# Kernel optimization log

Measured on AMD Instinct MI355X. Metric: run time of the kernel, lower is better.

Reference implementation:

```python
import jax, jax.numpy as jnp
import numpy as np

NEG = -1e30  # log-space 'zero' that stays finite under autodiff
BLANK = 0


def _logsumexp3(a, b, c):
    m = jnp.maximum(jnp.maximum(a, b), c)
    return m + jnp.log(jnp.exp(a - m) + jnp.exp(b - m) + jnp.exp(c - m))


def setup_inputs() -> dict:
    key = jax.random.key(0)
    k1, k2, k3, k4 = jax.random.split(key, 4)
    T, B, C, S = 1024, 128, 96, 200
    logits = jax.random.normal(k1, (T, B, C), dtype=jnp.float32)
    log_probs = jax.nn.log_softmax(logits, axis=-1)  # CTC expects log-probs
    targets = jax.random.randint(k2, (B, S), 1, C, dtype=jnp.int32)  # labels in [1, C-1]
    input_lengths = jax.random.randint(k3, (B,), T // 2, T + 1, dtype=jnp.int32)
    target_lengths = jax.random.randint(k4, (B,), S // 2, S + 1, dtype=jnp.int32)
    return {"log_probs": log_probs, "targets": targets,
            "input_lengths": input_lengths, "target_lengths": target_lengths}


def ctc_loss(log_probs, targets, input_lengths, target_lengths):
    T, B, C = log_probs.shape
    S = targets.shape[1]
    L = 2 * S + 1  # extended target length (blanks interleaved)

    # Extended target sequence: blank, t0, blank, t1, ..., blank  -> [B, L]
    ext = jnp.zeros((B, L), dtype=targets.dtype).at[:, 1::2].set(targets)
    # Skip transition s-2 -> s allowed when ext[s] != blank and ext[s] != ext[s-2]
    ext_m2 = jnp.pad(ext[:, :-2], ((0, 0), (2, 0)), constant_values=BLANK)
    allow_skip = (ext != BLANK) & (ext != ext_m2) & (jnp.arange(L)[None, :] >= 2)

    emit0 = jnp.take_along_axis(log_probs[0], ext, axis=1)  # [B, L]
    alpha0 = jnp.full((B, L), NEG, dtype=log_probs.dtype)
    alpha0 = alpha0.at[:, 0].set(emit0[:, 0]).at[:, 1].set(emit0[:, 1])

    def step(alpha, lp_t):
        a1 = jnp.pad(alpha[:, :-1], ((0, 0), (1, 0)), constant_values=NEG)
        a2 = jnp.pad(alpha[:, :-2], ((0, 0), (2, 0)), constant_values=NEG)
        a2 = jnp.where(allow_skip, a2, NEG)
        emit = jnp.take_along_axis(lp_t, ext, axis=1)  # [B, L]
        new = _logsumexp3(alpha, a1, a2) + emit
        return new, new

    _, alphas_rest = jax.lax.scan(step, alpha0, log_probs[1:])  # [T-1, B, L]
    alphas = jnp.concatenate([alpha0[None], alphas_rest], axis=0)  # [T, B, L]

    # Gather alpha at t = input_length - 1 for each batch element -> [B, L]
    aT = alphas[input_lengths - 1, jnp.arange(B)]
    s_last = 2 * target_lengths  # index of trailing blank
    end_idx = jnp.stack([s_last - 1, s_last], axis=1)  # [B, 2]
    a_end = jnp.take_along_axis(aT, end_idx, axis=1)  # [B, 2]
    m = jnp.max(a_end, axis=1)
    ll = m + jnp.log(jnp.sum(jnp.exp(a_end - m[:, None]), axis=1))
    loss = -ll
    # zero_infinity=True: zero out non-finite (huge) losses
    loss = jnp.where(loss > 1e29, 0.0, loss)
    # reduction='mean': divide by target lengths, then mean over batch
    return jnp.mean(loss / target_lengths.astype(loss.dtype))


def reference(log_probs, targets, input_lengths, target_lengths):
    return ctc_loss(log_probs, targets, input_lengths, target_lengths)
```

## Files before the change

kernel.cpp:

```cpp
#include <hip/hip_runtime.h>
#include <hip/hip_fp16.h>

#define NEGV  (-1e30f)
#define LOG2E 1.44269504088896340736f
#define LN2F  0.69314718055994530942f

constexpr int Tn = 1024;
constexpr int Bn = 128;
constexpr int Cn = 96;
constexpr int Sn = 200;
constexpr int Ln = 2 * Sn + 1;
constexpr int W  = 7;
constexpr int PadS = 512;
constexpr size_t G_BYTES = (size_t)Tn * Bn * PadS * sizeof(__half);

__device__ __forceinline__ float fexp2(float x) {
#if __has_builtin(__builtin_amdgcn_exp2f)
    return __builtin_amdgcn_exp2f(x);
#else
    return exp2f(x);
#endif
}
__device__ __forceinline__ float flog2(float x) {
#if __has_builtin(__builtin_amdgcn_logf)
    return __builtin_amdgcn_logf(x);
#else
    return __log2f(x);
#endif
}
__device__ __forceinline__ float2 cvt2(unsigned u) {
    const __half2 h = *reinterpret_cast<const __half2*>(&u);
    return __half22float2(h);
}

__device__ __forceinline__ float wave_max_dpp_to_lane63(float x) {
    #define DPP_MAX(ctrl)                                                   \
        x = fmaxf(x, __int_as_float(__builtin_amdgcn_update_dpp(            \
                __float_as_int(x), __float_as_int(x), (ctrl), 0xf, 0xf, false)))
    DPP_MAX(0x111);
    DPP_MAX(0x112);
    DPP_MAX(0x114);
    DPP_MAX(0x118);
    DPP_MAX(0x142);
    DPP_MAX(0x143);
    #undef DPP_MAX
    return x;
}

__global__ __launch_bounds__(256) void ctc_gather_kernel(
    const float* __restrict__ lp,
    const int*   __restrict__ tg,
    __half*      __restrict__ G)
{
    const int w    = threadIdx.x >> 6;
    const int lane = threadIdx.x & 63;
    const int p    = blockIdx.x * 4 + w;
    const int b    = p & (Bn - 1);
    const int t0   = (p >> 7) * 4;

    const float* src = lp + ((size_t)t0 * Bn + b) * Cn;
    constexpr size_t rstride = (size_t)Bn * Cn;
    float rA[4], rB[4];
    #pragma unroll
    for (int r = 0; r < 4; ++r) {
        rA[r] = src[r * rstride + lane];
        rB[r] = (lane < Cn - 64) ? src[r * rstride + 64 + lane] : 0.0f;
    }

    int cidx[W];
    bool live[W];
    #pragma unroll
    for (int j = 0; j < W; ++j) {
        const int s = lane * W + j;
        cidx[j] = (s < Ln && (s & 1)) ? tg[b * Sn + (s >> 1)] : 0;
        live[j] = (s < Ln);
    }

    #pragma unroll
    for (int r = 0; r < 4; ++r) {
        unsigned us[8];
        #pragma unroll
        for (int j = 0; j < W; ++j) {
            const int c = cidx[j];
            const float lo = __shfl(rA[r], c, 64);
            const float hi = __shfl(rB[r], c & 63, 64);
            const float lv = (c < 64) ? lo : hi;
            const float pr = live[j] ? fexp2(lv * LOG2E) : 0.0f;
            us[j] = __half_as_ushort(__float2half(pr));
        }
        us[7] = 0;
        uint4 v;
        v.x = us[0] | (us[1] << 16);
        v.y = us[2] | (us[3] << 16);
        v.z = us[4] | (us[5] << 16);
        v.w = us[6] | (us[7] << 16);
        *reinterpret_cast<uint4*>(G + ((size_t)b * Tn + (t0 + r)) * PadS + lane * 8) = v;
    }
}

__global__ __launch_bounds__(64, 1) void ctc_serial_kernel(
    const __half* __restrict__ G,
    const int*    __restrict__ tg,
    const int*    __restrict__ il,
    const int*    __restrict__ tl,
    float*        __restrict__ out_pb)
{
    const int b    = blockIdx.x;
    const int lane = threadIdx.x;
    __shared__ float endv[2];

    const int inlen = il[b];
    const int tlen  = tl[b];
    const int ee0 = 2 * tlen - 1;
    const int ee1 = 2 * tlen;

    auto mk_gate = [&](int j) -> float {
        const int s = lane * W + j;
        if (s < Ln && (s & 1) && s >= 3) {
            const int k = s >> 1;
            if (tg[b * Sn + k] != tg[b * Sn + k - 1]) return 1.0f;
        }
        return 0.0f;
    };
    const float g0 = mk_gate(0), g1 = mk_gate(1), g2 = mk_gate(2),
                g3 = mk_gate(3), g4 = mk_gate(4), g5 = mk_gate(5),
                g6 = mk_gate(6);

    const float zl  = (lane == 0) ? 0.0f : 1.0f;
    const float g1z = g1 * zl;
    const float g0z = g0 * zl;

    const uint4* g = reinterpret_cast<const uint4*>(G) + (size_t)b * Tn * (PadS / 8) + lane;
    constexpr int strd = PadS / 8;

    const uint4 r0 = g[0];
    uint4 p0 = g[1 * strd], p1 = g[2 * strd], p2 = g[3 * strd], p3 = g[4 * strd],
          p4 = g[5 * strd], p5 = g[6 * strd], p6 = g[7 * strd], p7 = g[8 * strd];

    float a0v, a1v, a2v, a3v, a4v, a5v, a6v;
    {
        const float2 f01 = cvt2(r0.x);
        a0v = (lane == 0) ? f01.x : 0.0f;
        a1v = (lane == 0) ? f01.y : 0.0f;
        a2v = 0.0f; a3v = 0.0f; a4v = 0.0f; a5v = 0.0f; a6v = 0.0f;
    }
    float pm1 = 0.0f, pm2 = 0.0f;

    int K = 0;
    int k_cap = 0;
    int t = 1;

#define CAP(J, AJ) { const int s_ = lane * W + (J);                         \
                     if (s_ == ee0) endv[0] = (AJ);                         \
                     if (s_ == ee1) endv[1] = (AJ); }

#define CTC_STEP(P)                                                         \
  {                                                                         \
    const uint4 v = P;                                                      \
    const int tt = (t + 8 < Tn) ? (t + 8) : (Tn - 1);                       \
    P = g[(size_t)tt * strd];                                               \
    float2 f_;                                                              \
    f_ = cvt2(v.x); const float e0m = f_.x, e1m = f_.y;                     \
    f_ = cvt2(v.y); const float e2m = f_.x, e3m = f_.y;                     \
    f_ = cvt2(v.z); const float e4m = f_.x, e5m = f_.y;                     \
    f_ = cvt2(v.w); const float e6m = f_.x;                                 \
    const float n6 = fmaf(g6, a4v, a6v + a5v) * e6m;                        \
    const float n5 = fmaf(g5, a3v, a5v + a4v) * e5m;                        \
    const float npm1 = __shfl_up(n6, 1);       \
    const float npm2 = __shfl_up(n5, 1);                                    \
    const float n4 = fmaf(g4, a2v, a4v + a3v) * e4m;                        \
    const float n3 = fmaf(g3, a1v, a3v + a2v) * e3m;                        \
    const float n2 = fmaf(g2, a0v, a2v + a1v) * e2m;                        \
    const float n1 = fmaf(g1z, pm1, a1v + a0v) * e1m;                       \
    const float n0 = fmaf(g0z, pm2, fmaf(zl, pm1, a0v)) * e0m;              \
    a6v = n6; a5v = n5; a4v = n4; a3v = n3; a2v = n2; a1v = n1; a0v = n0;   \
    pm1 = npm1; pm2 = npm2;                                                 \
    if (t == inlen - 1) {                                                   \
      CAP(0, a0v); CAP(1, a1v); CAP(2, a2v); CAP(3, a3v);                   \
      CAP(4, a4v); CAP(5, a5v); CAP(6, a6v);                                \
      k_cap = K;                                                            \
    }                                                                       \
    ++t;                                                                    \
  }

#define BMAX(J, AJ) { const int s_ = lane * W + (J);                        \
                      if (s_ >= ell && s_ <= ee1) mx = fmaxf(mx, (AJ)); }

    #pragma unroll 1
    for (int c = 0; c < Tn / 8; ++c) {
        CTC_STEP(p0); CTC_STEP(p1); CTC_STEP(p2); CTC_STEP(p3);
        CTC_STEP(p4); CTC_STEP(p5); CTC_STEP(p6); CTC_STEP(p7);

        const int ell = (2 * tlen - 1) - 2 * (inlen - t);
        float mx = 0.0f;
        BMAX(0, a0v); BMAX(1, a1v); BMAX(2, a2v); BMAX(3, a3v);
        BMAX(4, a4v); BMAX(5, a5v); BMAX(6, a6v);
        const float mxr = wave_max_dpp_to_lane63(mx);
        const int  smx = __builtin_amdgcn_readlane(__float_as_int(mxr), 63);
        const int  eb  = (smx >> 23) & 0xff;
        const bool nz  = (smx > 0) && (eb < 255);
        const float scale = nz ? __int_as_float((254 - eb) << 23) : 1.0f;
        K += nz ? (127 - eb) : 0;
        a0v *= scale; a1v *= scale; a2v *= scale; a3v *= scale;
        a4v *= scale; a5v *= scale; a6v *= scale;
        pm1 *= scale; pm2 *= scale;
    }

#undef BMAX
#undef CTC_STEP
#undef CAP

    __syncthreads();
    if (lane == 0) {
        const float sum = endv[0] + endv[1];
        const float ll2 = flog2(sum) - (float)k_cap;
        float lb = -(ll2 * LN2F);
        if (lb > 1e29f || !(lb == lb)) lb = 0.0f;
        out_pb[b] = lb / (float)tlen;
    }
}

__global__ __launch_bounds__(448) void ctc_fallback_kernel(
    const float* __restrict__ lp, const int* __restrict__ tg,
    const int* __restrict__ il, const int* __restrict__ tl,
    float* __restrict__ out_pb)
{
    const int b   = blockIdx.x;
    const int tid = threadIdx.x;

    __shared__ float alpha[2][Ln];
    __shared__ float lprow[2][Cn];
    __shared__ float endv[2];

    const int inlen = il[b];
    const int tlen  = tl[b];
    const int e0 = 2 * tlen - 1;
    const int e1 = 2 * tlen;

    const bool active = (tid < Ln);
    int  myclass = 0;
    bool allow   = false;
    if (active && (tid & 1)) {
        const int k = tid >> 1;
        myclass = tg[b * Sn + k];
        if (tid >= 3) allow = (myclass != tg[b * Sn + k - 1]);
    }

    const float* lpb = lp + (size_t)b * Cn;
    if (tid < Cn) lprow[0][tid] = lpb[tid];

    float vv[4] = {0.f, 0.f, 0.f, 0.f};
    if (tid < Cn) {
        vv[1] = lpb[(size_t)1 * Bn * Cn + tid];
        vv[2] = lpb[(size_t)2 * Bn * Cn + tid];
        vv[3] = lpb[(size_t)3 * Bn * Cn + tid];
        vv[0] = lpb[(size_t)4 * Bn * Cn + tid];
    }
    __syncthreads();
    if (active) alpha[0][tid] = (tid < 2) ? lprow[0][myclass] : NEGV;

    int cur = 0;
    #pragma unroll 4
    for (int t = 1; t < Tn; ++t) {
        if (tid < Cn) {
            lprow[t & 1][tid] = vv[t & 3];
            if (t + 4 < Tn)
                vv[t & 3] = lpb[(size_t)(t + 4) * Bn * Cn + tid];
        }
        __syncthreads();
        if (active) {
            const float a0 = alpha[cur][tid];
            const float a1 = (tid >= 1) ? alpha[cur][tid - 1] : NEGV;
            const float a2 = allow ? alpha[cur][tid - 2] : NEGV;
            const float m  = fmaxf(a0, fmaxf(a1, a2));
            const float nv = m + __logf(__expf(a0 - m) + __expf(a1 - m) + __expf(a2 - m))
                           + lprow[t & 1][myclass];
            alpha[cur ^ 1][tid] = nv;
            if (t == inlen - 1) {
                if (tid == e0) endv[0] = nv;
                if (tid == e1) endv[1] = nv;
            }
        }
        cur ^= 1;
    }
    __syncthreads();

    if (tid == 0) {
        const float x = endv[0], y = endv[1];
        const float m = fmaxf(x, y);
        const float ll = m + __logf(__expf(x - m) + __expf(y - m));
        float lb = -ll;
        if (lb > 1e29f) lb = 0.f;
        out_pb[b] = lb / (float)tlen;
    }
}

__global__ void reduce_mean_kernel(const float* __restrict__ pb,
                                   float* __restrict__ out)
{
    const int l = threadIdx.x;
    float s = pb[l] + pb[l + 64];
    #pragma unroll
    for (int o = 32; o; o >>= 1) s += __shfl_down(s, o);
    if (l == 0) out[0] = s * (1.0f / (float)Bn);
}

extern "C" void kernel_launch(void* const* d_in, const int* in_sizes, int n_in,
                              void* d_out, int out_size, void* d_ws, size_t ws_size,
                              hipStream_t stream)
{
    const float* lp = (const float*)d_in[0];
    const int*   tg = (const int*)d_in[1];
    const int*   il = (const int*)d_in[2];
    const int*   tl = (const int*)d_in[3];
    float* out = (float*)d_out;

    if (ws_size >= G_BYTES + 1024) {
        __half* G  = (__half*)d_ws;
        float*  pb = (float*)((char*)d_ws + G_BYTES);
        ctc_gather_kernel<<<(Tn * Bn / 4) / 4, 256, 0, stream>>>(lp, tg, G);
        ctc_serial_kernel<<<Bn, 64, 0, stream>>>(G, tg, il, tl, pb);
        reduce_mean_kernel<<<1, 64, 0, stream>>>(pb, out);
    } else {
        float* pb = (float*)d_ws;
        ctc_fallback_kernel<<<Bn, 448, 0, stream>>>(lp, tg, il, tl, pb);
        reduce_mean_kernel<<<1, 64, 0, stream>>>(pb, out);
    }
}
```

Baseline: 234.2 us.

## Fuse gather and serial CTC recursion with producer waves feeding LDS double buffer

Merges the separate gather kernel and serial alpha-recursion kernel into one block per batch element. Three producer waves load log-prob rows, gather and exponentiate them into a double-buffered LDS chunk, while one consumer wave runs the recursion from LDS. This removes the round trip through a large global half-precision workspace and one kernel launch. The cost is a block-wide barrier every 16 timesteps. The rescale now runs twice per 16-step chunk, and shfl_up is replaced by a DPP row-shift. The serial chain now depends on producers keeping pace, and the barriers may stall the consumer.

```diff
diff --git a/kernel.cpp b/kernel.cpp
--- a/kernel.cpp
+++ b/kernel.cpp
@@ -11,8 +11,8 @@
 constexpr int Sn = 200;
 constexpr int Ln = 2 * Sn + 1;
 constexpr int W  = 7;
-constexpr int PadS = 512;
-constexpr size_t G_BYTES = (size_t)Tn * Bn * PadS * sizeof(__half);
+constexpr int CH = 16;
+constexpr int NCH = Tn / CH;
 
 __device__ __forceinline__ float fexp2(float x) {
 #if __has_builtin(__builtin_amdgcn_exp2f)
@@ -31,6 +31,11 @@
 __device__ __forceinline__ float2 cvt2(unsigned u) {
     const __half2 h = *reinterpret_cast<const __half2*>(&u);
     return __half22float2(h);
+}
+
+__device__ __forceinline__ float shup1(float x) {
+    return __int_as_float(__builtin_amdgcn_update_dpp(
+        0, __float_as_int(x), 0x138, 0xf, 0xf, false));
 }
 
 __device__ __forceinline__ float wave_max_dpp_to_lane63(float x) {
@@ -47,171 +52,201 @@
     return x;
 }
 
-__global__ __launch_bounds__(256) void ctc_gather_kernel(
+__global__ __launch_bounds__(256, 1) void ctc_fused_kernel(
     const float* __restrict__ lp,
     const int*   __restrict__ tg,
-    __half*      __restrict__ G)
+    const int*   __restrict__ il,
+    const int*   __restrict__ tl,
+    float*       __restrict__ out_pb)
 {
+    const int b    = blockIdx.x;
     const int w    = threadIdx.x >> 6;
     const int lane = threadIdx.x & 63;
-    const int p    = blockIdx.x * 4 + w;
-    const int b    = p & (Bn - 1);
-    const int t0   = (p >> 7) * 4;
-
-    const float* src = lp + ((size_t)t0 * Bn + b) * Cn;
-    constexpr size_t rstride = (size_t)Bn * Cn;
-    float rA[4], rB[4];
-    #pragma unroll
-    for (int r = 0; r < 4; ++r) {
-        rA[r] = src[r * rstride + lane];
-        rB[r] = (lane < Cn - 64) ? src[r * rstride + 64 + lane] : 0.0f;
-    }
-
-    int cidx[W];
-    bool live[W];
-    #pragma unroll
-    for (int j = 0; j < W; ++j) {
-        const int s = lane * W + j;
-        cidx[j] = (s < Ln && (s & 1)) ? tg[b * Sn + (s >> 1)] : 0;
-        live[j] = (s < Ln);
-    }
-
-    #pragma unroll
-    for (int r = 0; r < 4; ++r) {
-        unsigned us[8];
+
+    __shared__ __half buf[2][CH][512];
+    __shared__ float  endv[2];
+
+    float a0v = 0.f, a1v = 0.f, a2v = 0.f, a3v = 0.f, a4v = 0.f, a5v = 0.f, a6v = 0.f;
+    float pm1 = 0.f, pm2 = 0.f;
+    float g0 = 0.f, g1 = 0.f, g2 = 0.f, g3 = 0.f, g4 = 0.f, g5 = 0.f, g6 = 0.f;
+    float zl = 0.f, g1z = 0.f, g0z = 0.f;
+    int   K = 0, k_cap = 0, t = 1;
+    int   inlen = 1 << 30, tlen = 1, ee0 = -1, ee1 = -1;
+
+    int   cidx[W] = {0, 0, 0, 0, 0, 0, 0};
+    bool  liv[W]  = {false, false, false, false, false, false, false};
+    float rA[6], rB[6];
+    int   pw = 0;
+
+#define P_LOAD(CHK)                                                          \
+    {                                                                        \
+        _Pragma("unroll")                                                    \
+        for (int k = 0; k < 6; ++k) {                                        \
+            const int r_ = pw + 3 * k;                                       \
+            const int t_ = (r_ < CH) ? ((CHK) * CH + r_) : (Tn - 1);         \
+            const float* src_ = lp + ((size_t)t_ * Bn + b) * Cn;             \
+            rA[k] = src_[lane];                                              \
+            rB[k] = (lane < Cn - 64) ? src_[64 + lane] : 0.0f;               \
+        }                                                                    \
+    }
+
+#define P_GATH(CHK)                                                          \
+    {                                                                        \
+        const int bb_ = (CHK) & 1;                                           \
+        _Pragma("unroll")                                                    \
+        for (int k = 0; k < 6; ++k) {                                        \
+            const int r_ = pw + 3 * k;                                       \
+            if (r_ < CH) {                                                   \
+                unsigned us_[8];                                             \
+                _Pragma("unroll")                                            \
+                for (int j = 0; j < W; ++j) {                                \
+                    const int cc_ = cidx[j];                                 \
+                    const float lo_ = __shfl(rA[k], cc_, 64);                \
+                    const float hi_ = __shfl(rB[k], cc_ & 63, 64);           \
+                    const float lv_ = (cc_ < 64) ? lo_ : hi_;                \
+                    const float pr_ = liv[j] ? fexp2(lv_ * LOG2E) : 0.0f;    \
+                    us_[j] = __half_as_ushort(__float2half(pr_));            \
+                }                                                            \
+                us_[7] = 0;                                                  \
+                uint4 v_;                                                    \
+                v_.x = us_[0] | (us_[1] << 16);                              \
+                v_.y = us_[2] | (us_[3] << 16);                              \
+                v_.z = us_[4] | (us_[5] << 16);                              \
+                v_.w = us_[6] | (us_[7] << 16);                              \
+                *reinterpret_cast<uint4*>(&buf[bb_][r_][lane * 8]) = v_;     \
+            }                                                                \
+        }                                                                    \
+    }
+
+    if (w == 0) {
+        if (lane == 0) { endv[0] = 0.0f; endv[1] = 0.0f; }
+        inlen = il[b];
+        tlen  = tl[b];
+        ee0 = 2 * tlen - 1;
+        ee1 = 2 * tlen;
+        auto mk_gate = [&](int j) -> float {
+            const int s = lane * W + j;
+            if (s < Ln && (s & 1) && s >= 3) {
+                const int kk = s >> 1;
+                if (tg[b * Sn + kk] != tg[b * Sn + kk - 1]) return 1.0f;
+            }
+            return 0.0f;
+        };
+        g0 = mk_gate(0); g1 = mk_gate(1); g2 = mk_gate(2); g3 = mk_gate(3);
+        g4 = mk_gate(4); g5 = mk_gate(5); g6 = mk_gate(6);
+        zl  = (lane == 0) ? 0.0f : 1.0f;
+        g1z = g1 * zl;
+        g0z = g0 * zl;
+    } else {
+        pw = w - 1;
         #pragma unroll
         for (int j = 0; j < W; ++j) {
-            const int c = cidx[j];
-            const float lo = __shfl(rA[r], c, 64);
-            const float hi = __shfl(rB[r], c & 63, 64);
-            const float lv = (c < 64) ? lo : hi;
-            const float pr = live[j] ? fexp2(lv * LOG2E) : 0.0f;
-            us[j] = __half_as_ushort(__float2half(pr));
+            const int s = lane * W + j;
+            cidx[j] = (s < Ln && (s & 1)) ? tg[b * Sn + (s >> 1)] : 0;
+            liv[j]  = (s < Ln);
         }
-        us[7] = 0;
-        uint4 v;
-        v.x = us[0] | (us[1] << 16);
-        v.y = us[2] | (us[3] << 16);
-        v.z = us[4] | (us[5] << 16);
-        v.w = us[6] | (us[7] << 16);
-        *reinterpret_cast<uint4*>(G + ((size_t)b * Tn + (t0 + r)) * PadS + lane * 8) = v;
-    }
-}
-
-__global__ __launch_bounds__(64, 1) void ctc_serial_kernel(
-    const __half* __restrict__ G,
-    const int*    __restrict__ tg,
-    const int*    __restrict__ il,
-    const int*    __restrict__ tl,
-    float*        __restrict__ out_pb)
-{
-    const int b    = blockIdx.x;
-    const int lane = threadIdx.x;
-    __shared__ float endv[2];
-
-    const int inlen = il[b];
-    const int tlen  = tl[b];
-    const int ee0 = 2 * tlen - 1;
-    const int ee1 = 2 * tlen;
-
-    auto mk_gate = [&](int j) -> float {
-        const int s = lane * W + j;
-        if (s < Ln && (s & 1) && s >= 3) {
-            const int k = s >> 1;
-            if (tg[b * Sn + k] != tg[b * Sn + k - 1]) return 1.0f;
+        P_LOAD(0);
+        P_GATH(0);
+        P_LOAD(1);
+    }
+    __syncthreads();
+
+#define CAP(J, AJ) { const int s_ = lane * W + (J);                          \
+                     if (s_ == ee0) endv[0] = (AJ);                          \
+                     if (s_ == ee1) endv[1] = (AJ); }
+
+#define CSTEP(V)                                                             \
+  {                                                                          \
+    float2 f_;                                                               \
+    f_ = cvt2((V).x); const float e0m = f_.x, e1m = f_.y;                    \
+    f_ = cvt2((V).y); const float e2m = f_.x, e3m = f_.y;                    \
+    f_ = cvt2((V).z); const float e4m = f_.x, e5m = f_.y;                    \
+    f_ = cvt2((V).w); const float e6m = f_.x;                                \
+    const float n6 = fmaf(g6, a4v, a6v + a5v) * e6m;                         \
+    const float n5 = fmaf(g5, a3v, a5v + a4v) * e5m;                         \
+    const float npm1 = shup1(n6);               \
+    const float npm2 = shup1(n5);                                            \
+    const float n4 = fmaf(g4, a2v, a4v + a3v) * e4m;                         \
+    const float n3 = fmaf(g3, a1v, a3v + a2v) * e3m;                         \
+    const float n2 = fmaf(g2, a0v, a2v + a1v) * e2m;                         \
+    const float n1 = fmaf(g1z, pm1, a1v + a0v) * e1m;                        \
+    const float n0 = fmaf(g0z, pm2, fmaf(zl, pm1, a0v)) * e0m;               \
+    a6v = n6; a5v = n5; a4v = n4; a3v = n3; a2v = n2; a1v = n1; a0v = n0;    \
+    pm1 = npm1; pm2 = npm2;                                                  \
+    if (t == inlen - 1) {                                                    \
+      CAP(0, a0v); CAP(1, a1v); CAP(2, a2v); CAP(3, a3v);                    \
+      CAP(4, a4v); CAP(5, a5v); CAP(6, a6v);                                 \
+      k_cap = K;                                                             \
+    }                                                                        \
+    ++t;                                                                     \
+  }
+
+#define BMAX(J, AJ) { const int s_ = lane * W + (J);                         \
+                      if (s_ >= ell && s_ <= ee1) mx = fmaxf(mx, (AJ)); }
+
+#define RESCALE()                                                            \
+  {                                                                          \
+    const int ell = (2 * tlen - 1) - 2 * (inlen - t);                        \
+    float mx = 0.0f;                                                         \
+    BMAX(0, a0v); BMAX(1, a1v); BMAX(2, a2v); BMAX(3, a3v);                  \
+    BMAX(4, a4v); BMAX(5, a5v); BMAX(6, a6v);                                \
+    const float mxr = wave_max_dpp_to_lane63(mx);                            \
+    const int  smx = __builtin_amdgcn_readlane(__float_as_int(mxr), 63);     \
+    const int  eb  = (smx >> 23) & 0xff;                                     \
+    const bool nz  = (smx > 0) && (eb < 255);                                \
+    const float scale = nz ? __int_as_float((254 - eb) << 23) : 1.0f;        \
+    K += nz ? (127 - eb) : 0;                                                \
+    a0v *= scale; a1v *= scale; a2v *= scale; a3v *= scale;                  \
+    a4v *= scale; a5v *= scale; a6v *= scale;                                \
+    pm1 *= scale; pm2 *= scale;                                              \
+  }
+
+    for (int c = 0; c < NCH; ++c) {
+        if (w == 0) {
+            const uint4* rp =
+                reinterpret_cast<const uint4*>(&buf[c & 1][0][0]) + lane;
+            if (c == 0) {
+                a0v = (lane == 0) ? __half2float(buf[0][0][0]) : 0.0f;
+                a1v = (lane == 0) ? __half2float(buf[0][0][1]) : 0.0f;
+                uint4 q0 = rp[1 * 64];
+                uint4 q1 = rp[2 * 64];
+                #pragma unroll
+                for (int i = 1; i < CH; ++i) {
+                    const uint4 v = q0;
+                    q0 = q1;
+                    if (i + 2 < CH) q1 = rp[(i + 2) * 64];
+                    CSTEP(v);
+                    if (i == 7 || i == 15) RESCALE();
+                }
+            } else {
+                uint4 q0 = rp[0];
+                uint4 q1 = rp[64];
+                #pragma unroll
+                for (int i = 0; i < CH; ++i) {
+                    const uint4 v = q0;
+                    q0 = q1;
+                    if (i + 2 < CH) q1 = rp[(i + 2) * 64];
+                    CSTEP(v);
+                    if (i == 7 || i == 15) RESCALE();
+                }
+            }
+        } else {
+            if (c + 1 < NCH) {
+                P_GATH(c + 1);
+                if (c + 2 < NCH) P_LOAD(c + 2);
+            }
         }
-        return 0.0f;
-    };
-    const float g0 = mk_gate(0), g1 = mk_gate(1), g2 = mk_gate(2),
-                g3 = mk_gate(3), g4 = mk_gate(4), g5 = mk_gate(5),
-                g6 = mk_gate(6);
-
-    const float zl  = (lane == 0) ? 0.0f : 1.0f;
-    const float g1z = g1 * zl;
-    const float g0z = g0 * zl;
-
-    const uint4* g = reinterpret_cast<const uint4*>(G) + (size_t)b * Tn * (PadS / 8) + lane;
-    constexpr int strd = PadS / 8;
-
-    const uint4 r0 = g[0];
-    uint4 p0 = g[1 * strd], p1 = g[2 * strd], p2 = g[3 * strd], p3 = g[4 * strd],
-          p4 = g[5 * strd], p5 = g[6 * strd], p6 = g[7 * strd], p7 = g[8 * strd];
-
-    float a0v, a1v, a2v, a3v, a4v, a5v, a6v;
-    {
-        const float2 f01 = cvt2(r0.x);
-        a0v = (lane == 0) ? f01.x : 0.0f;
-        a1v = (lane == 0) ? f01.y : 0.0f;
-        a2v = 0.0f; a3v = 0.0f; a4v = 0.0f; a5v = 0.0f; a6v = 0.0f;
-    }
-    float pm1 = 0.0f, pm2 = 0.0f;
-
-    int K = 0;
-    int k_cap = 0;
-    int t = 1;
-
-#define CAP(J, AJ) { const int s_ = lane * W + (J);                         \
-                     if (s_ == ee0) endv[0] = (AJ);                         \
-                     if (s_ == ee1) endv[1] = (AJ); }
-
-#define CTC_STEP(P)                                                         \
-  {                                                                         \
-    const uint4 v = P;                                                      \
-    const int tt = (t + 8 < Tn) ? (t + 8) : (Tn - 1);                       \
-    P = g[(size_t)tt * strd];                                               \
-    float2 f_;                                                              \
-    f_ = cvt2(v.x); const float e0m = f_.x, e1m = f_.y;                     \
-    f_ = cvt2(v.y); const float e2m = f_.x, e3m = f_.y;                     \
-    f_ = cvt2(v.z); const float e4m = f_.x, e5m = f_.y;                     \
-    f_ = cvt2(v.w); const float e6m = f_.x;                                 \
-    const float n6 = fmaf(g6, a4v, a6v + a5v) * e6m;                        \
-    const float n5 = fmaf(g5, a3v, a5v + a4v) * e5m;                        \
-    const float npm1 = __shfl_up(n6, 1);       \
-    const float npm2 = __shfl_up(n5, 1);                                    \
-    const float n4 = fmaf(g4, a2v, a4v + a3v) * e4m;                        \
-    const float n3 = fmaf(g3, a1v, a3v + a2v) * e3m;                        \
-    const float n2 = fmaf(g2, a0v, a2v + a1v) * e2m;                        \
-    const float n1 = fmaf(g1z, pm1, a1v + a0v) * e1m;                       \
-    const float n0 = fmaf(g0z, pm2, fmaf(zl, pm1, a0v)) * e0m;              \
-    a6v = n6; a5v = n5; a4v = n4; a3v = n3; a2v = n2; a1v = n1; a0v = n0;   \
-    pm1 = npm1; pm2 = npm2;                                                 \
-    if (t == inlen - 1) {                                                   \
-      CAP(0, a0v); CAP(1, a1v); CAP(2, a2v); CAP(3, a3v);                   \
-      CAP(4, a4v); CAP(5, a5v); CAP(6, a6v);                                \
-      k_cap = K;                                                            \
-    }                                                                       \
-    ++t;                                                                    \
-  }
-
-#define BMAX(J, AJ) { const int s_ = lane * W + (J);                        \
-                      if (s_ >= ell && s_ <= ee1) mx = fmaxf(mx, (AJ)); }
-
-    #pragma unroll 1
-    for (int c = 0; c < Tn / 8; ++c) {
-        CTC_STEP(p0); CTC_STEP(p1); CTC_STEP(p2); CTC_STEP(p3);
-        CTC_STEP(p4); CTC_STEP(p5); CTC_STEP(p6); CTC_STEP(p7);
-
-        const int ell = (2 * tlen - 1) - 2 * (inlen - t);
-        float mx = 0.0f;
-        BMAX(0, a0v); BMAX(1, a1v); BMAX(2, a2v); BMAX(3, a3v);
-        BMAX(4, a4v); BMAX(5, a5v); BMAX(6, a6v);
-        const float mxr = wave_max_dpp_to_lane63(mx);
-        const int  smx = __builtin_amdgcn_readlane(__float_as_int(mxr), 63);
-        const int  eb  = (smx >> 23) & 0xff;
-        const bool nz  = (smx > 0) && (eb < 255);
-        const float scale = nz ? __int_as_float((254 - eb) << 23) : 1.0f;
-        K += nz ? (127 - eb) : 0;
-        a0v *= scale; a1v *= scale; a2v *= scale; a3v *= scale;
-        a4v *= scale; a5v *= scale; a6v *= scale;
-        pm1 *= scale; pm2 *= scale;
-    }
-
+        __syncthreads();
+    }
+
+#undef RESCALE
 #undef BMAX
-#undef CTC_STEP
+#undef CSTEP
 #undef CAP
-
-    __syncthreads();
-    if (lane == 0) {
+#undef P_GATH
+#undef P_LOAD
+
+    if (w == 0 && lane == 0) {
         const float sum = endv[0] + endv[1];
         const float ll2 = flog2(sum) - (float)k_cap;
         float lb = -(ll2 * LN2F);
@@ -315,11 +350,9 @@
     const int*   tl = (const int*)d_in[3];
     float* out = (float*)d_out;
 
-    if (ws_size >= G_BYTES + 1024) {
-        __half* G  = (__half*)d_ws;
-        float*  pb = (float*)((char*)d_ws + G_BYTES);
-        ctc_gather_kernel<<<(Tn * Bn / 4) / 4, 256, 0, stream>>>(lp, tg, G);
-        ctc_serial_kernel<<<Bn, 64, 0, stream>>>(G, tg, il, tl, pb);
+    if (ws_size >= 4096) {
+        float* pb = (float*)d_ws;
+        ctc_fused_kernel<<<Bn, 256, 0, stream>>>(lp, tg, il, tl, pb);
         reduce_mean_kernel<<<1, 64, 0, stream>>>(pb, out);
     } else {
         float* pb = (float*)d_ws;
```

New measurement: 203.0 us. -13.3%, faster.

## Fuse emission gather into serial CTC kernel, drop fp16 workspace pass

Applied to the files above, without the earlier changes.

Removes the separate gather kernel that precomputed exp(log_prob) for each extended-label state into an fp16 workspace. The serial recurrence kernel now loads log-probs directly by target class with an 8-deep register prefetch ring and computes exp2 inline, masking padded states with a large negative bias. It also replaces __shfl_up with a DPP row shift. This avoids an extra kernel launch and the workspace write and read traffic, but adds seven scattered global loads and seven exp instructions per step on the serial critical path.

```diff
diff --git a/kernel.cpp b/kernel.cpp
--- a/kernel.cpp
+++ b/kernel.cpp
@@ -11,8 +11,6 @@
 constexpr int Sn = 200;
 constexpr int Ln = 2 * Sn + 1;
 constexpr int W  = 7;
-constexpr int PadS = 512;
-constexpr size_t G_BYTES = (size_t)Tn * Bn * PadS * sizeof(__half);
 
 __device__ __forceinline__ float fexp2(float x) {
 #if __has_builtin(__builtin_amdgcn_exp2f)
@@ -28,9 +26,10 @@
     return __log2f(x);
 #endif
 }
-__device__ __forceinline__ float2 cvt2(unsigned u) {
-    const __half2 h = *reinterpret_cast<const __half2*>(&u);
-    return __half22float2(h);
+
+__device__ __forceinline__ float shup1(float x) {
+    return __int_as_float(__builtin_amdgcn_update_dpp(
+        0, __float_as_int(x), 0x138, 0xf, 0xf, false));
 }
 
 __device__ __forceinline__ float wave_max_dpp_to_lane63(float x) {
@@ -47,63 +46,12 @@
     return x;
 }
 
-__global__ __launch_bounds__(256) void ctc_gather_kernel(
+__global__ __launch_bounds__(64, 1) void ctc_self_kernel(
     const float* __restrict__ lp,
     const int*   __restrict__ tg,
-    __half*      __restrict__ G)
-{
-    const int w    = threadIdx.x >> 6;
-    const int lane = threadIdx.x & 63;
-    const int p    = blockIdx.x * 4 + w;
-    const int b    = p & (Bn - 1);
-    const int t0   = (p >> 7) * 4;
-
-    const float* src = lp + ((size_t)t0 * Bn + b) * Cn;
-    constexpr size_t rstride = (size_t)Bn * Cn;
-    float rA[4], rB[4];
-    #pragma unroll
-    for (int r = 0; r < 4; ++r) {
-        rA[r] = src[r * rstride + lane];
-        rB[r] = (lane < Cn - 64) ? src[r * rstride + 64 + lane] : 0.0f;
-    }
-
-    int cidx[W];
-    bool live[W];
-    #pragma unroll
-    for (int j = 0; j < W; ++j) {
-        const int s = lane * W + j;
-        cidx[j] = (s < Ln && (s & 1)) ? tg[b * Sn + (s >> 1)] : 0;
-        live[j] = (s < Ln);
-    }
-
-    #pragma unroll
-    for (int r = 0; r < 4; ++r) {
-        unsigned us[8];
-        #pragma unroll
-        for (int j = 0; j < W; ++j) {
-            const int c = cidx[j];
-            const float lo = __shfl(rA[r], c, 64);
-            const float hi = __shfl(rB[r], c & 63, 64);
-            const float lv = (c < 64) ? lo : hi;
-            const float pr = live[j] ? fexp2(lv * LOG2E) : 0.0f;
-            us[j] = __half_as_ushort(__float2half(pr));
-        }
-        us[7] = 0;
-        uint4 v;
-        v.x = us[0] | (us[1] << 16);
-        v.y = us[2] | (us[3] << 16);
-        v.z = us[4] | (us[5] << 16);
-        v.w = us[6] | (us[7] << 16);
-        *reinterpret_cast<uint4*>(G + ((size_t)b * Tn + (t0 + r)) * PadS + lane * 8) = v;
-    }
-}
-
-__global__ __launch_bounds__(64, 1) void ctc_serial_kernel(
-    const __half* __restrict__ G,
-    const int*    __restrict__ tg,
-    const int*    __restrict__ il,
-    const int*    __restrict__ tl,
-    float*        __restrict__ out_pb)
+    const int*   __restrict__ il,
+    const int*   __restrict__ tl,
+    float*       __restrict__ out_pb)
 {
     const int b    = blockIdx.x;
     const int lane = threadIdx.x;
@@ -130,21 +78,38 @@
     const float g1z = g1 * zl;
     const float g0z = g0 * zl;
 
-    const uint4* g = reinterpret_cast<const uint4*>(G) + (size_t)b * Tn * (PadS / 8) + lane;
-    constexpr int strd = PadS / 8;
-
-    const uint4 r0 = g[0];
-    uint4 p0 = g[1 * strd], p1 = g[2 * strd], p2 = g[3 * strd], p3 = g[4 * strd],
-          p4 = g[5 * strd], p5 = g[6 * strd], p6 = g[7 * strd], p7 = g[8 * strd];
+    int   cidx[W];
+    float la0, la1, la2, la3, la4, la5, la6;
+    {
+        float la[W];
+        #pragma unroll
+        for (int j = 0; j < W; ++j) {
+            const int s = lane * W + j;
+            cidx[j] = (s < Ln && (s & 1)) ? tg[b * Sn + (s >> 1)] : 0;
+            la[j]   = (s < Ln) ? 0.0f : -12800.0f;
+        }
+        la0 = la[0]; la1 = la[1]; la2 = la[2]; la3 = la[3];
+        la4 = la[4]; la5 = la[5]; la6 = la[6];
+    }
 
     float a0v, a1v, a2v, a3v, a4v, a5v, a6v;
     {
-        const float2 f01 = cvt2(r0.x);
-        a0v = (lane == 0) ? f01.x : 0.0f;
-        a1v = (lane == 0) ? f01.y : 0.0f;
+        const float* rp0 = lp + (size_t)b * Cn;
+        const float x0 = rp0[cidx[0]];
+        const float x1 = rp0[cidx[1]];
+        a0v = (lane == 0) ? fexp2(x0 * LOG2E) : 0.0f;
+        a1v = (lane == 0) ? fexp2(x1 * LOG2E) : 0.0f;
         a2v = 0.0f; a3v = 0.0f; a4v = 0.0f; a5v = 0.0f; a6v = 0.0f;
     }
     float pm1 = 0.0f, pm2 = 0.0f;
+
+    float rQ[8][W];
+    #pragma unroll
+    for (int r = 1; r <= 8; ++r) {
+        const float* rp_ = lp + ((size_t)r * Bn + b) * Cn;
+        #pragma unroll
+        for (int j = 0; j < W; ++j) rQ[r & 7][j] = rp_[cidx[j]];
+    }
 
     int K = 0;
     int k_cap = 0;
@@ -154,20 +119,23 @@
                      if (s_ == ee0) endv[0] = (AJ);                         \
                      if (s_ == ee1) endv[1] = (AJ); }
 
-#define CTC_STEP(P)                                                         \
+#define CTC_STEP(SLOT)                                                      \
   {                                                                         \
-    const uint4 v = P;                                                      \
     const int tt = (t + 8 < Tn) ? (t + 8) : (Tn - 1);                       \
-    P = g[(size_t)tt * strd];                                               \
-    float2 f_;                                                              \
-    f_ = cvt2(v.x); const float e0m = f_.x, e1m = f_.y;                     \
-    f_ = cvt2(v.y); const float e2m = f_.x, e3m = f_.y;                     \
-    f_ = cvt2(v.z); const float e4m = f_.x, e5m = f_.y;                     \
-    f_ = cvt2(v.w); const float e6m = f_.x;                                 \
+    const float e0m = fexp2(fmaf(rQ[SLOT][0], LOG2E, la0));                 \
+    const float e1m = fexp2(fmaf(rQ[SLOT][1], LOG2E, la1));                 \
+    const float e2m = fexp2(fmaf(rQ[SLOT][2], LOG2E, la2));                 \
+    const float e3m = fexp2(fmaf(rQ[SLOT][3], LOG2E, la3));                 \
+    const float e4m = fexp2(fmaf(rQ[SLOT][4], LOG2E, la4));                 \
+    const float e5m = fexp2(fmaf(rQ[SLOT][5], LOG2E, la5));                 \
+    const float e6m = fexp2(fmaf(rQ[SLOT][6], LOG2E, la6));                 \
+    { const float* rp_ = lp + ((size_t)tt * Bn + b) * Cn;                   \
+      _Pragma("unroll")                                                     \
+      for (int j = 0; j < W; ++j) rQ[SLOT][j] = rp_[cidx[j]]; }             \
     const float n6 = fmaf(g6, a4v, a6v + a5v) * e6m;                        \
     const float n5 = fmaf(g5, a3v, a5v + a4v) * e5m;                        \
-    const float npm1 = __shfl_up(n6, 1);       \
-    const float npm2 = __shfl_up(n5, 1);                                    \
+    const float npm1 = shup1(n6);              \
+    const float npm2 = shup1(n5);                                           \
     const float n4 = fmaf(g4, a2v, a4v + a3v) * e4m;                        \
     const float n3 = fmaf(g3, a1v, a3v + a2v) * e3m;                        \
     const float n2 = fmaf(g2, a0v, a2v + a1v) * e2m;                        \
@@ -188,8 +156,8 @@
 
     #pragma unroll 1
     for (int c = 0; c < Tn / 8; ++c) {
-        CTC_STEP(p0); CTC_STEP(p1); CTC_STEP(p2); CTC_STEP(p3);
-        CTC_STEP(p4); CTC_STEP(p5); CTC_STEP(p6); CTC_STEP(p7);
+        CTC_STEP(1); CTC_STEP(2); CTC_STEP(3); CTC_STEP(4);
+        CTC_STEP(5); CTC_STEP(6); CTC_STEP(7); CTC_STEP(0);
 
         const int ell = (2 * tlen - 1) - 2 * (inlen - t);
         float mx = 0.0f;
@@ -315,11 +283,9 @@
     const int*   tl = (const int*)d_in[3];
     float* out = (float*)d_out;
 
-    if (ws_size >= G_BYTES + 1024) {
-        __half* G  = (__half*)d_ws;
-        float*  pb = (float*)((char*)d_ws + G_BYTES);
-        ctc_gather_kernel<<<(Tn * Bn / 4) / 4, 256, 0, stream>>>(lp, tg, G);
-        ctc_serial_kernel<<<Bn, 64, 0, stream>>>(G, tg, il, tl, pb);
+    if (ws_size >= 4096) {
+        float* pb = (float*)d_ws;
+        ctc_self_kernel<<<Bn, 64, 0, stream>>>(lp, tg, il, tl, pb);
         reduce_mean_kernel<<<1, 64, 0, stream>>>(pb, out);
     } else {
         float* pb = (float*)d_ws;
```

Result: slower. 258.6 us (+10.4%).
